# Kernel tuning notes

Measured on AMD Instinct MI355X. Metric: run time of the kernel, lower is better.

The kernel has to match this reference:

```python
import jax, jax.numpy as jnp
import numpy as np

B, N, F_IN, F_OUT, H = 2, 4096, 256, 64, 4


def setup_inputs() -> dict:
    key = jax.random.key(0)
    k_adj, k_h, k_w, k_l, k_r = jax.random.split(key, 5)
    adj = jax.random.randint(k_adj, (B, N, N), 0, 2, dtype=jnp.int32)
    h = jax.random.normal(k_h, (B, N, F_IN), dtype=jnp.float32)
    # xavier-uniform-ish params
    lim_w = float(np.sqrt(6.0 / (F_IN + F_OUT)))
    W = jax.random.uniform(k_w, (F_IN, F_OUT), jnp.float32, -lim_w, lim_w)
    lim_a = float(np.sqrt(6.0 / (F_OUT + H)))
    Wl = jax.random.uniform(k_l, (H, F_OUT), jnp.float32, -lim_a, lim_a)  # attn_l.weight
    Wr = jax.random.uniform(k_r, (H, F_OUT), jnp.float32, -lim_a, lim_a)  # attn_r.weight
    b = jnp.zeros((F_OUT,), jnp.float32)
    return {"adj": adj, "h": h, "W": W, "Wl": Wl, "Wr": Wr, "b": b}


def reference(adj, h, W, Wl, Wr, b):
    # dropout layers are identity in eval mode
    x = jnp.einsum('bnf,fo->bno', h, W)                       # (B,N,F_OUT)
    el = jnp.einsum('bno,ho->bnh', x, Wl)                     # (B,N,H)
    er = jnp.einsum('bno,ho->bnh', x, Wr)                     # (B,N,H)
    attn = el[:, :, None, :] + er[:, None, :, :]              # (B,N,N,H)
    attn = jax.nn.leaky_relu(attn, negative_slope=0.2)
    attn = jnp.where(adj[..., None] == 0, -jnp.inf, attn)
    attn = jax.nn.softmax(attn, axis=2)                       # softmax over source nodes j
    out = jnp.einsum('bijh,bjf->bihf', attn, x)               # (B,N,H,F_OUT)
    out = out + b                                             # bias over feature dim
    out = jax.nn.elu(out)                                     # activation
    return out.reshape(B, N, H * F_OUT)                       # n_heads>1 concat; B>1 keeps batch
```

## Files before the change

### kernel.cpp

```cpp
#include <hip/hip_runtime.h>
#include <hip/hip_bf16.h>


#define NN 4096
#define NH 4
#define JT 128
#define NT (NN / JT)
#define LOG2E 1.4426950408889634f

typedef __bf16 bf16x8 __attribute__((ext_vector_type(8)));
typedef unsigned short ushortx8 __attribute__((ext_vector_type(8)));
typedef unsigned short us4 __attribute__((ext_vector_type(4)));
typedef float f32x4 __attribute__((ext_vector_type(4)));

__device__ __forceinline__ void gload_lds16(const void* g, void* lds) {
  __builtin_amdgcn_global_load_lds(
      (const __attribute__((address_space(1))) void*)g,
      (__attribute__((address_space(3))) void*)lds, 16, 0, 0);
}

__device__ __forceinline__ unsigned short f2bf(float x) {
  __hip_bfloat16 hb = __float2bfloat16(x);
  return __builtin_bit_cast(unsigned short, hb);
}

#if __has_builtin(__builtin_amdgcn_exp2f)
#define EXP2F(x) __builtin_amdgcn_exp2f(x)
#else
#define EXP2F(x) exp2f(x)
#endif

__global__ __launch_bounds__(256, 2) void gat_prep(
    const float* __restrict__ hmat, const float* __restrict__ W,
    const float* __restrict__ Wl, const float* __restrict__ Wr,
    unsigned short* __restrict__ xT, float* __restrict__ elT,
    float* __restrict__ erT)
{
  __shared__ __align__(16) float h_s[16][256];
  __shared__ float x_s[16][65];
  __shared__ float wlr_s[512];

  const int t  = threadIdx.x;
  const int wv = t >> 6;
  const int l  = t & 63;
  const int b  = blockIdx.x >> 8;
  const int i0 = (blockIdx.x & 255) << 4;

  {
    const float4* hsrc = (const float4*)(hmat + ((size_t)(b * NN + i0)) * 256);
    float4* hdst = (float4*)&h_s[0][0];
#pragma unroll
    for (int u = 0; u < 4; ++u) hdst[t + 256 * u] = hsrc[t + 256 * u];
    wlr_s[t]       = Wl[t];
    wlr_s[256 + t] = Wr[t];
  }
  __syncthreads();

  const int row0 = wv << 2;
  float acc[4] = {0.f, 0.f, 0.f, 0.f};
#pragma unroll 4
  for (int k4 = 0; k4 < 64; ++k4) {
    const float w0 = W[(k4 * 4 + 0) * 64 + l];
    const float w1 = W[(k4 * 4 + 1) * 64 + l];
    const float w2 = W[(k4 * 4 + 2) * 64 + l];
    const float w3 = W[(k4 * 4 + 3) * 64 + l];
#pragma unroll
    for (int rr = 0; rr < 4; ++rr) {
      const float4 hv = *(const float4*)&h_s[row0 + rr][k4 * 4];
      acc[rr] = fmaf(hv.x, w0, acc[rr]);
      acc[rr] = fmaf(hv.y, w1, acc[rr]);
      acc[rr] = fmaf(hv.z, w2, acc[rr]);
      acc[rr] = fmaf(hv.w, w3, acc[rr]);
    }
  }
#pragma unroll
  for (int rr = 0; rr < 4; ++rr) x_s[row0 + rr][l] = acc[rr];
  __syncthreads();

  if (t < 64) {
    const int row = t >> 2, hh = t & 3;
    float el = 0.f, er = 0.f;
#pragma unroll 8
    for (int f = 0; f < 64; ++f) {
      const float xv = x_s[row][f];
      el = fmaf(xv, wlr_s[hh * 64 + f], el);
      er = fmaf(xv, wlr_s[256 + hh * 64 + f], er);
    }
    elT[((size_t)b * NH + hh) * NN + i0 + row] = el * LOG2E;
    erT[((size_t)b * NH + hh) * NN + i0 + row] = er * LOG2E;
  }

  {
    const int f = t >> 2, q = t & 3;
    us4 pk;
#pragma unroll
    for (int rj = 0; rj < 4; ++rj) pk[rj] = f2bf(x_s[q * 4 + rj][f]);
    *(us4*)&xT[((size_t)(b * 64 + f)) * NN + i0 + q * 4] = pk;
  }
}

__global__ __launch_bounds__(256, 2) void gat_main(
    const int* __restrict__ adj, const unsigned short* __restrict__ xT,
    const float* __restrict__ elT, const float* __restrict__ erT,
    const float* __restrict__ bias, float* __restrict__ out)
{
  __shared__ __align__(16) int            adj_lds[3][16 * JT];
  __shared__ __align__(16) unsigned short xt_lds[3][64 * JT];
  __shared__ __align__(16) float          er_lds[3][NH * JT];

  const int t = threadIdx.x;
  const int w = t >> 6;
  const int l = t & 63;
  const int b  = blockIdx.x >> 8;
  const int i0 = (blockIdx.x & 255) << 4;

  const int lrow = l & 15;
  const int lk   = l >> 4;

  const float el_reg = elT[((size_t)b * NH + w) * NN + i0 + lrow];

  auto issue_tile = [&](int j0, int s) {
#pragma unroll
    for (int g = 0; g < 2; ++g) {
      const int gi  = w * 2 + g;
      const int row = gi * 2 + (l >> 5);
      const int src = ((l & 31) ^ (row & 7)) << 2;
      gload_lds16(adj + ((size_t)(b * NN + i0 + row)) * NN + j0 + src,
                  &adj_lds[s][gi * 256]);
    }
#pragma unroll
    for (int g = 0; g < 4; ++g) {
      const int gi = w * 4 + g;
      const int f  = gi * 4 + (l >> 4);
      const int src = ((l & 15) ^ (f & 7)) << 3;
      gload_lds16(xT + ((size_t)(b * 64 + f)) * NN + j0 + src,
                  &xt_lds[s][gi * 512]);
    }
    if (w >= 2) {
      const int h2 = (w - 2) * 2 + (l >> 5);
      gload_lds16(erT + ((size_t)b * NH + h2) * NN + j0 + ((l & 31) << 2),
                  &er_lds[s][(w - 2) * 256]);
    }
  };

  f32x4 acc[4] = {};
  f32x4 accd = {};
  ushortx8 ones_u;
#pragma unroll
  for (int i = 0; i < 8; ++i) ones_u[i] = 0x3F80;
  const bf16x8 onesf = __builtin_bit_cast(bf16x8, ones_u);

  issue_tile(0, 0);
  issue_tile(JT, 1);

  for (int it = 0; it < NT; ++it) {
    const int s = it % 3;
    if (it == NT - 1)  asm volatile("s_waitcnt vmcnt(0)" ::: "memory");
    else if (w < 2)    asm volatile("s_waitcnt vmcnt(6)" ::: "memory");
    else               asm volatile("s_waitcnt vmcnt(7)" ::: "memory");
    __builtin_amdgcn_s_barrier();
    __builtin_amdgcn_sched_barrier(0);

    if (it + 2 < NT) issue_tile((it + 2) * JT, (it + 2) % 3);

#pragma unroll
    for (int kc = 0; kc < 4; ++kc) {
      const int cbase = kc * 32 + (lk << 3);
      const int cq    = cbase >> 2;
      const int4 aj0 = *(const int4*)&adj_lds[s][lrow * JT + ((cq ^ (lrow & 7)) << 2)];
      const int4 aj1 = *(const int4*)&adj_lds[s][lrow * JT + (((cq + 1) ^ (lrow & 7)) << 2)];
      const float4 er0 = *(const float4*)&er_lds[s][w * JT + cbase];
      const float4 er1 = *(const float4*)&er_lds[s][w * JT + cbase + 4];

      ushortx8 pa;
#define SCORE(A_, E_, IDX) { \
        float s_  = el_reg + (E_); \
        float lr_ = fmaxf(s_, 0.2f * s_); \
        float w_  = (A_) ? EXP2F(lr_) : 0.0f; \
        pa[IDX] = f2bf(w_); }
      SCORE(aj0.x, er0.x, 0) SCORE(aj0.y, er0.y, 1)
      SCORE(aj0.z, er0.z, 2) SCORE(aj0.w, er0.w, 3)
      SCORE(aj1.x, er1.x, 4) SCORE(aj1.y, er1.y, 5)
      SCORE(aj1.z, er1.z, 6) SCORE(aj1.w, er1.w, 7)
#undef SCORE

      const bf16x8 A = __builtin_bit_cast(bf16x8, pa);
      accd = __builtin_amdgcn_mfma_f32_16x16x32_bf16(A, onesf, accd, 0, 0, 0);
#pragma unroll
      for (int fq = 0; fq < 4; ++fq) {
        const int f  = (fq << 4) + lrow;
        const int cb = (kc << 2) + lk;
        const int idx = f * JT + ((cb ^ (f & 7)) << 3);
        const bf16x8 Bf = __builtin_bit_cast(bf16x8, *(const ushortx8*)&xt_lds[s][idx]);
        acc[fq] = __builtin_amdgcn_mfma_f32_16x16x32_bf16(A, Bf, acc[fq], 0, 0, 0);
      }
    }
  }

  float inv[4];
#pragma unroll
  for (int r = 0; r < 4; ++r) inv[r] = 1.0f / accd[r];

#pragma unroll
  for (int fq = 0; fq < 4; ++fq) {
    const int f = (fq << 4) + lrow;
    const float bv = bias[f];
#pragma unroll
    for (int r = 0; r < 4; ++r) {
      const int ir = (lk << 2) + r;
      float v = acc[fq][r] * inv[r] + bv;
      v = v > 0.f ? v : (__expf(v) - 1.f);
      out[(((size_t)b * NN + i0 + ir) * NH + w) * 64 + f] = v;
    }
  }
}

extern "C" void kernel_launch(void* const* d_in, const int* in_sizes, int n_in,
                              void* d_out, int out_size, void* d_ws, size_t ws_size,
                              hipStream_t stream) {
  const int*   adj  = (const int*)d_in[0];
  const float* hmat = (const float*)d_in[1];
  const float* W    = (const float*)d_in[2];
  const float* Wl   = (const float*)d_in[3];
  const float* Wr   = (const float*)d_in[4];
  const float* bias = (const float*)d_in[5];
  float* out = (float*)d_out;

  unsigned short* xT = (unsigned short*)d_ws;
  float* elT = (float*)((char*)d_ws + (size_t)2 * 64 * NN * 2);
  float* erT = elT + (size_t)2 * NH * NN;

  gat_prep<<<512, 256, 0, stream>>>(hmat, W, Wl, Wr, xT, elT, erT);
  gat_main<<<512, 256, 0, stream>>>(adj, xT, elT, erT, bias, out);
}
```

Measured before the change: 248.6 us.

## Tile 64 rows per block with split-j partial sums and a finalize kernel

Each block now handles 64 query rows (four 16-row sets) over a quarter of the source range, so each xT tile loaded into LDS and registers is reused across four row sets instead of one. Partial numerators and denominators go either to per-quarter workspace buffers or, when the workspace is too small, into atomics on the output. A new finalize kernel sums the partials and applies normalization, bias and ELU. This costs extra global traffic for the partials, an extra launch, more accumulator registers, and possible memsets.

After: 251.3 us. Within noise of the previous version (+1.1%).

```diff
diff --git a/kernel.cpp b/kernel.cpp
--- a/kernel.cpp
+++ b/kernel.cpp
@@ -4,8 +4,11 @@
 
 #define NN 4096
 #define NH 4
-#define JT 128
-#define NT (NN / JT)
+#define JT 64
+#define IT 64
+#define NSET 4
+#define NJQ 4
+#define NTS ((NN / NJQ) / JT)
 #define LOG2E 1.4426950408889634f
 
 typedef __bf16 bf16x8 __attribute__((ext_vector_type(8)));
@@ -99,120 +102,193 @@
   }
 }
 
+template <bool ATOMIC>
 __global__ __launch_bounds__(256, 2) void gat_main(
     const int* __restrict__ adj, const unsigned short* __restrict__ xT,
     const float* __restrict__ elT, const float* __restrict__ erT,
-    const float* __restrict__ bias, float* __restrict__ out)
+    float* __restrict__ numP, float* __restrict__ denP)
 {
-  __shared__ __align__(16) int            adj_lds[3][16 * JT];
+  __shared__ __align__(16) int            adj_lds[3][IT * JT];
   __shared__ __align__(16) unsigned short xt_lds[3][64 * JT];
   __shared__ __align__(16) float          er_lds[3][NH * JT];
 
   const int t = threadIdx.x;
   const int w = t >> 6;
   const int l = t & 63;
-  const int b  = blockIdx.x >> 8;
-  const int i0 = (blockIdx.x & 255) << 4;
+  const int b     = blockIdx.x >> 8;
+  const int itile = (blockIdx.x & 255) >> 2;
+  const int jq    = blockIdx.x & 3;
+  const int i0    = itile << 6;
+  const int j0b   = jq << 10;
 
   const int lrow = l & 15;
   const int lk   = l >> 4;
 
-  const float el_reg = elT[((size_t)b * NH + w) * NN + i0 + lrow];
+  float el_reg[NSET];
+#pragma unroll
+  for (int set = 0; set < NSET; ++set)
+    el_reg[set] = elT[((size_t)b * NH + w) * NN + i0 + (set << 4) + lrow];
 
   auto issue_tile = [&](int j0, int s) {
 #pragma unroll
+    for (int g = 0; g < 4; ++g) {
+      const int gi = (w << 2) + g;
+      const int r  = (gi << 2) + (l >> 4);
+      gload_lds16(adj + ((size_t)(b * NN + i0 + r)) * NN + j0 +
+                      ((((l & 15) ^ (r & 7))) << 2),
+                  &adj_lds[s][gi << 8]);
+    }
+#pragma unroll
     for (int g = 0; g < 2; ++g) {
-      const int gi  = w * 2 + g;
-      const int row = gi * 2 + (l >> 5);
-      const int src = ((l & 31) ^ (row & 7)) << 2;
-      gload_lds16(adj + ((size_t)(b * NN + i0 + row)) * NN + j0 + src,
-                  &adj_lds[s][gi * 256]);
-    }
-#pragma unroll
-    for (int g = 0; g < 4; ++g) {
-      const int gi = w * 4 + g;
-      const int f  = gi * 4 + (l >> 4);
-      const int src = ((l & 15) ^ (f & 7)) << 3;
-      gload_lds16(xT + ((size_t)(b * 64 + f)) * NN + j0 + src,
-                  &xt_lds[s][gi * 512]);
-    }
-    if (w >= 2) {
-      const int h2 = (w - 2) * 2 + (l >> 5);
-      gload_lds16(erT + ((size_t)b * NH + h2) * NN + j0 + ((l & 31) << 2),
-                  &er_lds[s][(w - 2) * 256]);
+      const int gi = (w << 1) + g;
+      const int f  = (gi << 3) + (l >> 3);
+      gload_lds16(xT + ((size_t)(b * 64 + f)) * NN + j0 +
+                      ((((l & 7) ^ (f & 7))) << 3),
+                  &xt_lds[s][gi << 9]);
+    }
+    if (w == 3) {
+      const int h2 = l >> 4;
+      gload_lds16(erT + ((size_t)b * NH + h2) * NN + j0 + ((l & 15) << 2),
+                  &er_lds[s][0]);
     }
   };
 
-  f32x4 acc[4] = {};
-  f32x4 accd = {};
+  f32x4 acc[NSET][4] = {};
+  f32x4 accd[NSET] = {};
   ushortx8 ones_u;
 #pragma unroll
   for (int i = 0; i < 8; ++i) ones_u[i] = 0x3F80;
   const bf16x8 onesf = __builtin_bit_cast(bf16x8, ones_u);
 
-  issue_tile(0, 0);
-  issue_tile(JT, 1);
-
-  for (int it = 0; it < NT; ++it) {
+  issue_tile(j0b, 0);
+  issue_tile(j0b + JT, 1);
+
+  for (int it = 0; it < NTS; ++it) {
     const int s = it % 3;
-    if (it == NT - 1)  asm volatile("s_waitcnt vmcnt(0)" ::: "memory");
-    else if (w < 2)    asm volatile("s_waitcnt vmcnt(6)" ::: "memory");
+    if (it == NTS - 1) asm volatile("s_waitcnt vmcnt(0)" ::: "memory");
+    else if (w < 3)    asm volatile("s_waitcnt vmcnt(6)" ::: "memory");
     else               asm volatile("s_waitcnt vmcnt(7)" ::: "memory");
     __builtin_amdgcn_s_barrier();
     __builtin_amdgcn_sched_barrier(0);
 
-    if (it + 2 < NT) issue_tile((it + 2) * JT, (it + 2) % 3);
-
-#pragma unroll
-    for (int kc = 0; kc < 4; ++kc) {
-      const int cbase = kc * 32 + (lk << 3);
-      const int cq    = cbase >> 2;
-      const int4 aj0 = *(const int4*)&adj_lds[s][lrow * JT + ((cq ^ (lrow & 7)) << 2)];
-      const int4 aj1 = *(const int4*)&adj_lds[s][lrow * JT + (((cq + 1) ^ (lrow & 7)) << 2)];
-      const float4 er0 = *(const float4*)&er_lds[s][w * JT + cbase];
-      const float4 er1 = *(const float4*)&er_lds[s][w * JT + cbase + 4];
-
-      ushortx8 pa;
+    if (it + 2 < NTS) issue_tile(j0b + (it + 2) * JT, (it + 2) % 3);
+
+    float4 er_f[2][2];
+    bf16x8 Axt[2][4];
+#pragma unroll
+    for (int kc = 0; kc < 2; ++kc) {
+      er_f[kc][0] = *(const float4*)&er_lds[s][(w << 6) + (kc << 5) + (lk << 3)];
+      er_f[kc][1] = *(const float4*)&er_lds[s][(w << 6) + (kc << 5) + (lk << 3) + 4];
+#pragma unroll
+      for (int fq = 0; fq < 4; ++fq) {
+        const int f = (fq << 4) + lrow;
+        const int c = ((kc << 2) + lk) ^ (f & 7);
+        Axt[kc][fq] = __builtin_bit_cast(
+            bf16x8, *(const ushortx8*)&xt_lds[s][(f << 6) + (c << 3)]);
+      }
+    }
+
+#pragma unroll
+    for (int set = 0; set < NSET; ++set) {
+      const int r  = (set << 4) + lrow;
+      const int rb = r << 6;
+      const int sw = r & 7;
+#pragma unroll
+      for (int kc = 0; kc < 2; ++kc) {
+        const int cb = (kc << 3) + (lk << 1);
+        const int4 aj0 = *(const int4*)&adj_lds[s][rb + ((cb ^ sw) << 2)];
+        const int4 aj1 = *(const int4*)&adj_lds[s][rb + (((cb + 1) ^ sw) << 2)];
+        const float4 er0 = er_f[kc][0];
+        const float4 er1 = er_f[kc][1];
+
+        ushortx8 pa;
 #define SCORE(A_, E_, IDX) { \
-        float s_  = el_reg + (E_); \
+        float s_  = el_reg[set] + (E_); \
         float lr_ = fmaxf(s_, 0.2f * s_); \
         float w_  = (A_) ? EXP2F(lr_) : 0.0f; \
         pa[IDX] = f2bf(w_); }
-      SCORE(aj0.x, er0.x, 0) SCORE(aj0.y, er0.y, 1)
-      SCORE(aj0.z, er0.z, 2) SCORE(aj0.w, er0.w, 3)
-      SCORE(aj1.x, er1.x, 4) SCORE(aj1.y, er1.y, 5)
-      SCORE(aj1.z, er1.z, 6) SCORE(aj1.w, er1.w, 7)
+        SCORE(aj0.x, er0.x, 0) SCORE(aj0.y, er0.y, 1)
+        SCORE(aj0.z, er0.z, 2) SCORE(aj0.w, er0.w, 3)
+        SCORE(aj1.x, er1.x, 4) SCORE(aj1.y, er1.y, 5)
+        SCORE(aj1.z, er1.z, 6) SCORE(aj1.w, er1.w, 7)
 #undef SCORE
 
-      const bf16x8 A = __builtin_bit_cast(bf16x8, pa);
-      accd = __builtin_amdgcn_mfma_f32_16x16x32_bf16(A, onesf, accd, 0, 0, 0);
-#pragma unroll
-      for (int fq = 0; fq < 4; ++fq) {
-        const int f  = (fq << 4) + lrow;
-        const int cb = (kc << 2) + lk;
-        const int idx = f * JT + ((cb ^ (f & 7)) << 3);
-        const bf16x8 Bf = __builtin_bit_cast(bf16x8, *(const ushortx8*)&xt_lds[s][idx]);
-        acc[fq] = __builtin_amdgcn_mfma_f32_16x16x32_bf16(A, Bf, acc[fq], 0, 0, 0);
+        const bf16x8 P = __builtin_bit_cast(bf16x8, pa);
+        accd[set] = __builtin_amdgcn_mfma_f32_16x16x32_bf16(onesf, P, accd[set], 0, 0, 0);
+#pragma unroll
+        for (int fq = 0; fq < 4; ++fq)
+          acc[set][fq] = __builtin_amdgcn_mfma_f32_16x16x32_bf16(
+              Axt[kc][fq], P, acc[set][fq], 0, 0, 0);
       }
     }
   }
 
-  float inv[4];
-#pragma unroll
-  for (int r = 0; r < 4; ++r) inv[r] = 1.0f / accd[r];
-
-#pragma unroll
-  for (int fq = 0; fq < 4; ++fq) {
-    const int f = (fq << 4) + lrow;
-    const float bv = bias[f];
-#pragma unroll
-    for (int r = 0; r < 4; ++r) {
-      const int ir = (lk << 2) + r;
-      float v = acc[fq][r] * inv[r] + bv;
-      v = v > 0.f ? v : (__expf(v) - 1.f);
-      out[(((size_t)b * NN + i0 + ir) * NH + w) * 64 + f] = v;
-    }
-  }
+  if (ATOMIC) {
+#pragma unroll
+    for (int set = 0; set < NSET; ++set) {
+      const size_t obase = ((size_t)(b * NN + i0 + (set << 4) + lrow) * NH + w) << 6;
+#pragma unroll
+      for (int fq = 0; fq < 4; ++fq)
+#pragma unroll
+        for (int rr = 0; rr < 4; ++rr)
+          atomicAdd(&numP[obase + (fq << 4) + (lk << 2) + rr], acc[set][fq][rr]);
+    }
+    if (l < 16) {
+#pragma unroll
+      for (int set = 0; set < NSET; ++set)
+        atomicAdd(&denP[((size_t)(b * NN + i0 + (set << 4) + l)) * NH + w],
+                  accd[set][0]);
+    }
+  } else {
+    float* nb = numP + (size_t)jq * (2u * NN * NH * 64);
+#pragma unroll
+    for (int set = 0; set < NSET; ++set) {
+      const size_t obase = ((size_t)(b * NN + i0 + (set << 4) + lrow) * NH + w) << 6;
+#pragma unroll
+      for (int fq = 0; fq < 4; ++fq)
+        *(float4*)&nb[obase + (fq << 4) + (lk << 2)] = (float4){
+            acc[set][fq][0], acc[set][fq][1], acc[set][fq][2], acc[set][fq][3]};
+    }
+    if (l < 16) {
+      float* db = denP + (size_t)jq * (2u * NN * NH);
+#pragma unroll
+      for (int set = 0; set < NSET; ++set)
+        db[((size_t)(b * NN + i0 + (set << 4) + l)) * NH + w] = accd[set][0];
+    }
+  }
+}
+
+template <bool ATOMIC>
+__global__ __launch_bounds__(256) void gat_fin(
+    const float* __restrict__ numP, const float* __restrict__ denP,
+    const float* __restrict__ bias, float* __restrict__ out)
+{
+  const int g  = blockIdx.x * 256 + threadIdx.x;
+  const int f4 = (g & 15) << 2;
+  float4 n;
+  float d;
+  if (ATOMIC) {
+    n = *(const float4*)&out[(size_t)g * 4];
+    d = denP[g >> 4];
+  } else {
+    n = (float4){0.f, 0.f, 0.f, 0.f};
+    d = 0.f;
+#pragma unroll
+    for (int q = 0; q < NJQ; ++q) {
+      const float4 nq = *(const float4*)&numP[(size_t)q * (2u * NN * NH * 64) + (size_t)g * 4];
+      n.x += nq.x; n.y += nq.y; n.z += nq.z; n.w += nq.w;
+      d += denP[(size_t)q * (2u * NN * NH) + (g >> 4)];
+    }
+  }
+  const float inv = 1.0f / d;
+  const float4 bv = *(const float4*)&bias[f4];
+  float4 v = {n.x * inv + bv.x, n.y * inv + bv.y,
+              n.z * inv + bv.z, n.w * inv + bv.w};
+  v.x = v.x > 0.f ? v.x : (__expf(v.x) - 1.f);
+  v.y = v.y > 0.f ? v.y : (__expf(v.y) - 1.f);
+  v.z = v.z > 0.f ? v.z : (__expf(v.z) - 1.f);
+  v.w = v.w > 0.f ? v.w : (__expf(v.w) - 1.f);
+  *(float4*)&out[(size_t)g * 4] = v;
 }
 
 extern "C" void kernel_launch(void* const* d_in, const int* in_sizes, int n_in,
@@ -226,10 +302,23 @@
   const float* bias = (const float*)d_in[5];
   float* out = (float*)d_out;
 
-  unsigned short* xT = (unsigned short*)d_ws;
-  float* elT = (float*)((char*)d_ws + (size_t)2 * 64 * NN * 2);
-  float* erT = elT + (size_t)2 * NH * NN;
+  char* wsb = (char*)d_ws;
+  unsigned short* xT = (unsigned short*)wsb;
+  float* elT = (float*)(wsb + 1048576);
+  float* erT = (float*)(wsb + 1179648);
+  float* den = (float*)(wsb + 1310720);
+  float* num = (float*)(wsb + 1835008);
+  const bool partial = ws_size >= 35389440ull;
 
   gat_prep<<<512, 256, 0, stream>>>(hmat, W, Wl, Wr, xT, elT, erT);
-  gat_main<<<512, 256, 0, stream>>>(adj, xT, elT, erT, bias, out);
-}
+
+  if (partial) {
+    gat_main<false><<<512, 256, 0, stream>>>(adj, xT, elT, erT, num, den);
+    gat_fin<false><<<2048, 256, 0, stream>>>(num, den, bias, out);
+  } else {
+    hipMemsetAsync(out, 0, (size_t)out_size * 4, stream);
+    hipMemsetAsync(den, 0, 131072, stream);
+    gat_main<true><<<512, 256, 0, stream>>>(adj, xT, elT, erT, out, den);
+    gat_fin<true><<<2048, 256, 0, stream>>>(num, den, bias, out);
+  }
+}
```
